# Kernel tuning notes

Measured on AMD Instinct MI355X. Metric: run time of the kernel, lower is better.

## Reference

```python
import jax, jax.numpy as jnp
import numpy as np
import math

RADIUS = 32
NUM_HEADS = 8

B, L, DIM = 2, 8192, 256


def setup_inputs() -> dict:
    key = jax.random.key(0)
    k1, k2, k3, k4, k5 = jax.random.split(key, 5)
    s_in = 1.0 / math.sqrt(DIM)
    return {
        "x": jax.random.normal(k1, (B, L, DIM), dtype=jnp.float32),
        "w_qkv": jax.random.normal(k2, (DIM, 3 * DIM), dtype=jnp.float32) * s_in,
        "b_qkv": jax.random.normal(k3, (3 * DIM,), dtype=jnp.float32) * 0.01,
        "w_proj": jax.random.normal(k4, (DIM, DIM), dtype=jnp.float32) * s_in,
        "b_proj": jax.random.normal(k5, (DIM,), dtype=jnp.float32) * 0.01,
    }


def reference(x, w_qkv, b_qkv, w_proj, b_proj):
    B, L, dim = x.shape
    H = NUM_HEADS
    hd = dim // H
    R = RADIUS
    W = 2 * R + 1
    scale = math.sqrt(hd)

    qkv = x @ w_qkv + b_qkv                      # (B, L, 3*dim)
    qkv = qkv.reshape(B, L, 3, H, hd)
    qkv = jnp.transpose(qkv, (2, 0, 3, 1, 4))    # (3, B, H, L, hd)
    q = qkv[0].reshape(B * H, L, hd)
    k = qkv[1].reshape(B * H, L, hd)
    v = qkv[2].reshape(B * H, L, hd)

    # zero-pad along sequence (matches F.pad value=0: boundary windows attend
    # to zero vectors with logit 0, included in softmax)
    k_p = jnp.pad(k, ((0, 0), (R, R), (0, 0)))   # (BH, L+2R, hd)
    v_p = jnp.pad(v, ((0, 0), (R, R), (0, 0)))

    idx = jnp.arange(L)[:, None] + jnp.arange(W)[None, :]  # (L, W)
    k_w = k_p[:, idx]                            # (BH, L, W, hd)
    v_w = v_p[:, idx]                            # (BH, L, W, hd)

    scores = jnp.einsum('bld,blwd->blw', q, k_w) / scale
    attn = jax.nn.softmax(scores, axis=-1)
    out = jnp.einsum('blw,blwd->bld', attn, v_w)  # (BH, L, hd)

    out = out.reshape(B, H, L, hd)
    out = jnp.transpose(out, (0, 2, 1, 3)).reshape(B, L, dim)
    return out @ w_proj + b_proj
```

## Files before the change

### kernel.cpp

```cpp
#include <hip/hip_runtime.h>
#include <hip/hip_bf16.h>
#include <math.h>

#define B_SZ 2
#define L_SZ 8192
#define DIM 256
#define H_N 8
#define HD 32
#define RAD 32
#define M_ROWS (B_SZ * L_SZ)

typedef __bf16 bf16x8 __attribute__((ext_vector_type(8)));
typedef __bf16 bf16x4 __attribute__((ext_vector_type(4)));
typedef short  s16x4  __attribute__((ext_vector_type(4)));
typedef float  f32x4  __attribute__((ext_vector_type(4)));

typedef const __attribute__((address_space(1))) void gvoid_t;
typedef __attribute__((address_space(3))) void lvoid_t;

static __device__ __forceinline__ f32x4 mfma16_bf16(bf16x4 a, bf16x4 b, f32x4 c) {
#if __has_builtin(__builtin_amdgcn_mfma_f32_16x16x16bf16_1k)
    return __builtin_amdgcn_mfma_f32_16x16x16bf16_1k(
        __builtin_bit_cast(s16x4, a), __builtin_bit_cast(s16x4, b), c, 0, 0, 0);
#elif __has_builtin(__builtin_amdgcn_mfma_f32_16x16x16_bf16)
    return __builtin_amdgcn_mfma_f32_16x16x16_bf16(a, b, c, 0, 0, 0);
#else
    f32x4 d = c;
    asm volatile("v_mfma_f32_16x16x16_bf16 %0, %1, %2, %0\n\ts_nop 7\n\ts_nop 7"
                 : "+v"(d) : "v"(a), "v"(b));
    return d;
#endif
}

__global__ __launch_bounds__(256) void prep(const float* __restrict__ wq,
                                            const float* __restrict__ wp,
                                            __bf16* __restrict__ wqT,
                                            __bf16* __restrict__ wpT) {
    int idx = blockIdx.x * 256 + threadIdx.x;
    const int N2 = 3 * DIM * DIM;
    if (idx < N2) {
        int n = idx >> 8, k = idx & 255;
        wqT[idx] = (__bf16)wq[(size_t)k * (3 * DIM) + n];
    } else {
        int i3 = idx - N2;
        int n = i3 >> 8, k = i3 & 255;
        wpT[i3] = (__bf16)wp[(size_t)k * DIM + n];
    }
}

template<int BM, int BN, int WM, int WN, int N_DIM, int K_DIM, bool OUT_BF16, bool CAST_A>
__global__ __launch_bounds__(256) void gemm_bt(const void* __restrict__ Aptr,
                                               const __bf16* __restrict__ BT,
                                               const float* __restrict__ bias,
                                               void* __restrict__ Cout) {
    constexpr int BK = 32;
    constexpr int FM = BM / WM / 16;
    constexpr int FN = BN / WN / 16;
    __shared__ __bf16 As[BM * BK];
    __shared__ __bf16 Bs[BN * BK];
    const int tid = threadIdx.x;
    const int lane = tid & 63;
    const int wave = tid >> 6;
    const int wr = wave / WN;
    const int wc = wave % WN;
    const int row0 = blockIdx.y * BM;
    const int col0 = blockIdx.x * BN;

    f32x4 acc[FM][FN] = {};

    const int fr = lane & 15;
    const int fg = lane >> 4;

    for (int k0 = 0; k0 < K_DIM; k0 += BK) {
        #pragma unroll
        for (int i = 0; i < BN / 64; ++i) {
            int c  = tid + i * 256;
            int r  = c >> 2;
            int kk = (c & 3) * 8;
            __builtin_amdgcn_global_load_lds(
                (gvoid_t*)(BT + (size_t)(col0 + r) * K_DIM + (k0 + kk)),
                (lvoid_t*)(Bs + c * 8), 16, 0, 0);
        }
        if (CAST_A) {
            const float* Af = (const float*)Aptr;
            #pragma unroll
            for (int i = 0; i < BM / 64; ++i) {
                int c  = tid + i * 256;
                int r  = c >> 2;
                int kk = (c & 3) * 8;
                const float* ap = Af + (size_t)(row0 + r) * K_DIM + (k0 + kk);
                float4 v0 = *reinterpret_cast<const float4*>(ap);
                float4 v1 = *reinterpret_cast<const float4*>(ap + 4);
                bf16x8 w;
                w[0] = (__bf16)v0.x; w[1] = (__bf16)v0.y; w[2] = (__bf16)v0.z; w[3] = (__bf16)v0.w;
                w[4] = (__bf16)v1.x; w[5] = (__bf16)v1.y; w[6] = (__bf16)v1.z; w[7] = (__bf16)v1.w;
                *reinterpret_cast<bf16x8*>(As + c * 8) = w;
            }
        } else {
            const __bf16* Ab = (const __bf16*)Aptr;
            #pragma unroll
            for (int i = 0; i < BM / 64; ++i) {
                int c  = tid + i * 256;
                int r  = c >> 2;
                int kk = (c & 3) * 8;
                __builtin_amdgcn_global_load_lds(
                    (gvoid_t*)(Ab + (size_t)(row0 + r) * K_DIM + (k0 + kk)),
                    (lvoid_t*)(As + c * 8), 16, 0, 0);
            }
        }
        asm volatile("s_waitcnt vmcnt(0)" ::: "memory");
        __syncthreads();

        bf16x8 a[FM], b[FN];
        #pragma unroll
        for (int i = 0; i < FM; ++i)
            a[i] = *reinterpret_cast<const bf16x8*>(&As[(wr * (BM / WM) + i * 16 + fr) * BK + fg * 8]);
        #pragma unroll
        for (int j = 0; j < FN; ++j)
            b[j] = *reinterpret_cast<const bf16x8*>(&Bs[(wc * (BN / WN) + j * 16 + fr) * BK + fg * 8]);
        #pragma unroll
        for (int i = 0; i < FM; ++i)
            #pragma unroll
            for (int j = 0; j < FN; ++j)
                acc[i][j] = __builtin_amdgcn_mfma_f32_16x16x32_bf16(a[i], b[j], acc[i][j], 0, 0, 0);
        __syncthreads();
    }

    #pragma unroll
    for (int i = 0; i < FM; ++i) {
        #pragma unroll
        for (int j = 0; j < FN; ++j) {
            int cc = col0 + wc * (BN / WN) + j * 16 + fr;
            float bv = bias[cc];
            #pragma unroll
            for (int r = 0; r < 4; ++r) {
                int rr = row0 + wr * (BM / WM) + i * 16 + fg * 4 + r;
                float v = acc[i][j][r] + bv;
                if (OUT_BF16)
                    ((__bf16*)Cout)[(size_t)rr * N_DIM + cc] = (__bf16)v;
                else
                    ((float*)Cout)[(size_t)rr * N_DIM + cc] = v;
            }
        }
    }
}

__global__ __launch_bounds__(256) void natt_mfma(const __bf16* __restrict__ qkv,
                                                 __bf16* __restrict__ attn_out) {
    constexpr int VS = 216;
    __shared__ __bf16 vsT[32 * VS];

    const int tid  = threadIdx.x;
    const int lane = tid & 63;
    const int wave = tid >> 6;
    const int l15  = lane & 15;
    const int fg   = lane >> 4;
    const int bh = blockIdx.y;
    const int b  = bh >> 3;
    const int h  = bh & 7;
    const int bq0 = blockIdx.x * 128;
    const int wq0 = bq0 + wave * 32;

    const __bf16* base = qkv + (size_t)b * L_SZ * 768 + h * 32;

    #pragma unroll
    for (int i = 0; i < 3; ++i) {
        int c  = tid + i * 256;
        int sp = c >> 2;
        int dq = c & 3;
        int kp = bq0 - 32 + sp;
        bf16x8 v = {};
        if (kp >= 0 && kp < L_SZ)
            v = *reinterpret_cast<const bf16x8*>(base + (size_t)kp * 768 + 512 + dq * 8);
        int g = (sp >> 3) ^ dq;
        #pragma unroll
        for (int j = 0; j < 8; ++j)
            vsT[(dq * 8 + j) * VS + g * 8 + (sp & 7)] = v[j];
    }

    bf16x8 kf[6];
    #pragma unroll
    for (int t = 0; t < 6; ++t) {
        int kp = wq0 - 32 + t * 16 + l15;
        bf16x8 kv = {};
        if (kp >= 0 && kp < L_SZ)
            kv = *reinterpret_cast<const bf16x8*>(base + (size_t)kp * 768 + 256 + fg * 8);
        kf[t] = kv;
    }
    bf16x8 qf[2];
    #pragma unroll
    for (int s = 0; s < 2; ++s)
        qf[s] = *reinterpret_cast<const bf16x8*>(base + (size_t)(wq0 + s * 16 + l15) * 768 + fg * 8);

    __syncthreads();

    const float rscale = 0.17677669529663687f;

    #pragma unroll
    for (int s = 0; s < 2; ++s) {
        f32x4 st[5];
        __builtin_amdgcn_s_setprio(1);
        #pragma unroll
        for (int t = 0; t < 5; ++t)
            st[t] = __builtin_amdgcn_mfma_f32_16x16x32_bf16(kf[s + t], qf[s], f32x4{}, 0, 0, 0);
        __builtin_amdgcn_s_setprio(0);

        const int qr = l15;
        float sum = 0.f;
        #pragma unroll
        for (int t = 0; t < 5; ++t) {
            #pragma unroll
            for (int r = 0; r < 4; ++r) {
                int pr = 16 * t + 4 * fg + r;
                bool valid = (pr >= qr) && (pr <= qr + 64);
                float e = valid ? __expf(st[t][r] * rscale) : 0.f;
                st[t][r] = e;
                sum += e;
            }
        }
        sum += __shfl_xor(sum, 16);
        sum += __shfl_xor(sum, 32);
        float inv = 1.f / sum;

        bf16x4 pf[5];
        #pragma unroll
        for (int t = 0; t < 5; ++t) {
            bf16x4 p;
            #pragma unroll
            for (int r = 0; r < 4; ++r) p[r] = (__bf16)(st[t][r] * inv);
            pf[t] = p;
        }

        f32x4 acc[2] = {};
        __builtin_amdgcn_s_setprio(1);
        #pragma unroll
        for (int c = 0; c < 5; ++c) {
            #pragma unroll
            for (int dt = 0; dt < 2; ++dt) {
                int g = (4 * wave + 2 * s + 2 * c + (fg >> 1)) ^ (2 * dt + (l15 >> 3));
                bf16x4 vf = *reinterpret_cast<const bf16x4*>(
                    &vsT[(dt * 16 + l15) * VS + g * 8 + 4 * (fg & 1)]);
                acc[dt] = mfma16_bf16(pf[c], vf, acc[dt]);
            }
        }
        __builtin_amdgcn_s_setprio(0);

        __bf16* outp = attn_out + ((size_t)(b * L_SZ + wq0 + s * 16)) * 256 + h * 32;
        #pragma unroll
        for (int dt = 0; dt < 2; ++dt)
            #pragma unroll
            for (int r = 0; r < 4; ++r)
                outp[(size_t)(fg * 4 + r) * 256 + dt * 16 + l15] = (__bf16)acc[dt][r];
    }
}

extern "C" void kernel_launch(void* const* d_in, const int* in_sizes, int n_in,
                              void* d_out, int out_size, void* d_ws, size_t ws_size,
                              hipStream_t stream) {
    const float* x      = (const float*)d_in[0];
    const float* w_qkv  = (const float*)d_in[1];
    const float* b_qkv  = (const float*)d_in[2];
    const float* w_proj = (const float*)d_in[3];
    const float* b_proj = (const float*)d_in[4];
    float* out = (float*)d_out;

    __bf16* wqkvT  = (__bf16*)d_ws;
    __bf16* wprojT = wqkvT + (size_t)(3 * DIM) * DIM;
    __bf16* qkvb   = wprojT + (size_t)DIM * DIM;
    __bf16* ab     = qkvb  + (size_t)M_ROWS * (3 * DIM);

    prep<<<1024, 256, 0, stream>>>(w_qkv, w_proj, wqkvT, wprojT);

    dim3 g1(3 * DIM / 128, M_ROWS / 128);
    gemm_bt<128, 128, 2, 2, 3 * DIM, DIM, true, true><<<g1, 256, 0, stream>>>(x, wqkvT, b_qkv, qkvb);

    dim3 g2(L_SZ / 128, B_SZ * H_N);
    natt_mfma<<<g2, 256, 0, stream>>>(qkvb, ab);

    dim3 g3(DIM / 128, M_ROWS / 64);
    gemm_bt<64, 128, 1, 4, DIM, DIM, false, false><<<g3, 256, 0, stream>>>(ab, wprojT, b_proj, out);
}
```

Measured before the change: 49.73 us.

## Double-buffer GEMM tiles, load fp32 A via LDS DMA, swizzle blocks across XCDs

Gives the GEMM kernels double-buffered LDS so the next K-tile's global-to-LDS loads overlap the current tile's MFMAs. The fp32 input is now staged directly into LDS with global_load_lds and converted to bf16 when read, instead of going through registers. All three kernels use a 1D grid with an XCD-aware block swizzle to improve L2 locality, and the attention softmax uses exp2f with a prescaled constant. The cost is doubled LDS use, and twice the LDS bytes for the fp32 A tile, which may lower occupancy.

```diff
diff --git a/kernel.cpp b/kernel.cpp
--- a/kernel.cpp
+++ b/kernel.cpp
@@ -1,6 +1,7 @@
 #include <hip/hip_runtime.h>
 #include <hip/hip_bf16.h>
 #include <math.h>
+#include <type_traits>
 
 #define B_SZ 2
 #define L_SZ 8192
@@ -17,6 +18,10 @@
 
 typedef const __attribute__((address_space(1))) void gvoid_t;
 typedef __attribute__((address_space(3))) void lvoid_t;
+
+static __device__ __forceinline__ int xcd_swz(int id, int nwg) {
+    return (id & 7) * (nwg >> 3) + (id >> 3);
+}
 
 static __device__ __forceinline__ f32x4 mfma16_bf16(bf16x4 a, bf16x4 b, f32x4 c) {
 #if __has_builtin(__builtin_amdgcn_mfma_f32_16x16x16bf16_1k)
@@ -56,22 +61,49 @@
     constexpr int BK = 32;
     constexpr int FM = BM / WM / 16;
     constexpr int FN = BN / WN / 16;
-    __shared__ __bf16 As[BM * BK];
-    __shared__ __bf16 Bs[BN * BK];
+    constexpr int NT = K_DIM / BK;
+    constexpr int NBX = N_DIM / BN;
+    using AT = typename std::conditional<CAST_A, float, __bf16>::type;
+    __shared__ AT As[2][BM * BK];
+    __shared__ __bf16 Bs[2][BN * BK];
     const int tid = threadIdx.x;
     const int lane = tid & 63;
     const int wave = tid >> 6;
     const int wr = wave / WN;
     const int wc = wave % WN;
-    const int row0 = blockIdx.y * BM;
-    const int col0 = blockIdx.x * BN;
+    const int t0 = xcd_swz(blockIdx.x, gridDim.x);
+    const int row0 = (t0 / NBX) * BM;
+    const int col0 = (t0 % NBX) * BN;
 
     f32x4 acc[FM][FN] = {};
 
     const int fr = lane & 15;
     const int fg = lane >> 4;
 
-    for (int k0 = 0; k0 < K_DIM; k0 += BK) {
+    auto stage = [&](int buf, int k0) {
+        if (CAST_A) {
+            const float* Af = (const float*)Aptr;
+            #pragma unroll
+            for (int i = 0; i < BM * 8 / 256; ++i) {
+                int c  = tid + i * 256;
+                int r  = c >> 3;
+                int kk = (c & 7) * 4;
+                __builtin_amdgcn_global_load_lds(
+                    (gvoid_t*)(Af + (size_t)(row0 + r) * K_DIM + (k0 + kk)),
+                    (lvoid_t*)((float*)As[buf] + c * 4), 16, 0, 0);
+            }
+        } else {
+            const __bf16* Ab = (const __bf16*)Aptr;
+            #pragma unroll
+            for (int i = 0; i < BM / 64; ++i) {
+                int c  = tid + i * 256;
+                int r  = c >> 2;
+                int kk = (c & 3) * 8;
+                __builtin_amdgcn_global_load_lds(
+                    (gvoid_t*)(Ab + (size_t)(row0 + r) * K_DIM + (k0 + kk)),
+                    (lvoid_t*)((__bf16*)As[buf] + c * 8), 16, 0, 0);
+            }
+        }
         #pragma unroll
         for (int i = 0; i < BN / 64; ++i) {
             int c  = tid + i * 256;
@@ -79,52 +111,48 @@
             int kk = (c & 3) * 8;
             __builtin_amdgcn_global_load_lds(
                 (gvoid_t*)(BT + (size_t)(col0 + r) * K_DIM + (k0 + kk)),
-                (lvoid_t*)(Bs + c * 8), 16, 0, 0);
-        }
-        if (CAST_A) {
-            const float* Af = (const float*)Aptr;
-            #pragma unroll
-            for (int i = 0; i < BM / 64; ++i) {
-                int c  = tid + i * 256;
-                int r  = c >> 2;
-                int kk = (c & 3) * 8;
-                const float* ap = Af + (size_t)(row0 + r) * K_DIM + (k0 + kk);
-                float4 v0 = *reinterpret_cast<const float4*>(ap);
-                float4 v1 = *reinterpret_cast<const float4*>(ap + 4);
+                (lvoid_t*)(&Bs[buf][c * 8]), 16, 0, 0);
+        }
+    };
+    auto compute = [&](int buf) {
+        bf16x8 a[FM], b[FN];
+        #pragma unroll
+        for (int i = 0; i < FM; ++i) {
+            int rr = wr * (BM / WM) + i * 16 + fr;
+            if (CAST_A) {
+                const float* ap = (const float*)As[buf] + rr * BK + fg * 8;
+                f32x4 lo = *reinterpret_cast<const f32x4*>(ap);
+                f32x4 hi = *reinterpret_cast<const f32x4*>(ap + 4);
                 bf16x8 w;
-                w[0] = (__bf16)v0.x; w[1] = (__bf16)v0.y; w[2] = (__bf16)v0.z; w[3] = (__bf16)v0.w;
-                w[4] = (__bf16)v1.x; w[5] = (__bf16)v1.y; w[6] = (__bf16)v1.z; w[7] = (__bf16)v1.w;
-                *reinterpret_cast<bf16x8*>(As + c * 8) = w;
-            }
-        } else {
-            const __bf16* Ab = (const __bf16*)Aptr;
-            #pragma unroll
-            for (int i = 0; i < BM / 64; ++i) {
-                int c  = tid + i * 256;
-                int r  = c >> 2;
-                int kk = (c & 3) * 8;
-                __builtin_amdgcn_global_load_lds(
-                    (gvoid_t*)(Ab + (size_t)(row0 + r) * K_DIM + (k0 + kk)),
-                    (lvoid_t*)(As + c * 8), 16, 0, 0);
-            }
-        }
+                #pragma unroll
+                for (int j = 0; j < 4; ++j) { w[j] = (__bf16)lo[j]; w[j + 4] = (__bf16)hi[j]; }
+                a[i] = w;
+            } else {
+                a[i] = *reinterpret_cast<const bf16x8*>((const __bf16*)As[buf] + rr * BK + fg * 8);
+            }
+        }
+        #pragma unroll
+        for (int j = 0; j < FN; ++j)
+            b[j] = *reinterpret_cast<const bf16x8*>(&Bs[buf][(wc * (BN / WN) + j * 16 + fr) * BK + fg * 8]);
+        #pragma unroll
+        for (int i = 0; i < FM; ++i)
+            #pragma unroll
+            for (int j = 0; j < FN; ++j)
+                acc[i][j] = __builtin_amdgcn_mfma_f32_16x16x32_bf16(a[i], b[j], acc[i][j], 0, 0, 0);
+    };
+
+    stage(0, 0);
+    asm volatile("s_waitcnt vmcnt(0)" ::: "memory");
+    __syncthreads();
+    int cur = 0;
+    for (int t = 0; t < NT - 1; ++t) {
+        stage(cur ^ 1, (t + 1) * BK);
+        compute(cur);
         asm volatile("s_waitcnt vmcnt(0)" ::: "memory");
         __syncthreads();
-
-        bf16x8 a[FM], b[FN];
-        #pragma unroll
-        for (int i = 0; i < FM; ++i)
-            a[i] = *reinterpret_cast<const bf16x8*>(&As[(wr * (BM / WM) + i * 16 + fr) * BK + fg * 8]);
-        #pragma unroll
-        for (int j = 0; j < FN; ++j)
-            b[j] = *reinterpret_cast<const bf16x8*>(&Bs[(wc * (BN / WN) + j * 16 + fr) * BK + fg * 8]);
-        #pragma unroll
-        for (int i = 0; i < FM; ++i)
-            #pragma unroll
-            for (int j = 0; j < FN; ++j)
-                acc[i][j] = __builtin_amdgcn_mfma_f32_16x16x32_bf16(a[i], b[j], acc[i][j], 0, 0, 0);
-        __syncthreads();
-    }
+        cur ^= 1;
+    }
+    compute(cur);
 
     #pragma unroll
     for (int i = 0; i < FM; ++i) {
@@ -155,10 +183,11 @@
     const int wave = tid >> 6;
     const int l15  = lane & 15;
     const int fg   = lane >> 4;
-    const int bh = blockIdx.y;
+    const int t0 = xcd_swz(blockIdx.x, gridDim.x);
+    const int bh = t0 >> 6;
     const int b  = bh >> 3;
     const int h  = bh & 7;
-    const int bq0 = blockIdx.x * 128;
+    const int bq0 = (t0 & 63) * 128;
     const int wq0 = bq0 + wave * 32;
 
     const __bf16* base = qkv + (size_t)b * L_SZ * 768 + h * 32;
@@ -194,7 +223,7 @@
 
     __syncthreads();
 
-    const float rscale = 0.17677669529663687f;
+    const float cexp = 0.25501764f;
 
     #pragma unroll
     for (int s = 0; s < 2; ++s) {
@@ -213,7 +242,7 @@
             for (int r = 0; r < 4; ++r) {
                 int pr = 16 * t + 4 * fg + r;
                 bool valid = (pr >= qr) && (pr <= qr + 64);
-                float e = valid ? __expf(st[t][r] * rscale) : 0.f;
+                float e = valid ? exp2f(st[t][r] * cexp) : 0.f;
                 st[t][r] = e;
                 sum += e;
             }
@@ -271,12 +300,11 @@
 
     prep<<<1024, 256, 0, stream>>>(w_qkv, w_proj, wqkvT, wprojT);
 
-    dim3 g1(3 * DIM / 128, M_ROWS / 128);
-    gemm_bt<128, 128, 2, 2, 3 * DIM, DIM, true, true><<<g1, 256, 0, stream>>>(x, wqkvT, b_qkv, qkvb);
-
-    dim3 g2(L_SZ / 128, B_SZ * H_N);
-    natt_mfma<<<g2, 256, 0, stream>>>(qkvb, ab);
-
-    dim3 g3(DIM / 128, M_ROWS / 64);
-    gemm_bt<64, 128, 1, 4, DIM, DIM, false, false><<<g3, 256, 0, stream>>>(ab, wprojT, b_proj, out);
-}
+    gemm_bt<128, 128, 2, 2, 3 * DIM, DIM, true, true>
+        <<<(M_ROWS / 128) * (3 * DIM / 128), 256, 0, stream>>>(x, wqkvT, b_qkv, qkvb);
+
+    natt_mfma<<<(L_SZ / 128) * (B_SZ * H_N), 256, 0, stream>>>(qkvb, ab);
+
+    gemm_bt<64, 128, 1, 4, DIM, DIM, false, false>
+        <<<(M_ROWS / 64) * (DIM / 128), 256, 0, stream>>>(ab, wprojT, b_proj, out);
+}
```

After: 45.39 us, median of 2. -8.7%, faster.
